# Kernel tuning notes

Hardware: AMD Instinct MI355X
Metric: run time of the kernel (lower is better)

## Reference

```python
import jax, jax.numpy as jnp
import numpy as np

N_NODES = 100000
N_EDGES = 1600000
N_FEAT = 128
N_CLASSES = 64
K_HOPS = 2


def setup_inputs() -> dict:
    key = jax.random.key(0)
    k1, k2, k3 = jax.random.split(key, 3)
    x = jax.random.normal(k1, (N_NODES, N_FEAT), dtype=jnp.float32)
    edge_index = jax.random.randint(k2, (2, N_EDGES), 0, N_NODES, dtype=jnp.int64)
    # Linear layer params (PyG Linear: y = x @ W.T + b)
    lim = 1.0 / np.sqrt(N_FEAT)
    W = jax.random.uniform(k3, (N_CLASSES, N_FEAT), dtype=jnp.float32, minval=-lim, maxval=lim)
    b = jnp.zeros((N_CLASSES,), dtype=jnp.float32)
    return {"x": x, "edge_index": edge_index, "W": W, "b": b}


def _gcn_norm(edge_index, num_nodes):
    # Add self-loops with weight 1 (PyG gcn_norm default)
    loops = jnp.arange(num_nodes, dtype=edge_index.dtype)
    row = jnp.concatenate([edge_index[0], loops])
    col = jnp.concatenate([edge_index[1], loops])
    ew = jnp.ones(row.shape[0], dtype=jnp.float32)
    deg = jax.ops.segment_sum(ew, col, num_segments=num_nodes)
    dinv = jnp.where(deg > 0, jax.lax.rsqrt(deg), 0.0)
    norm = dinv[row] * ew * dinv[col]  # [E + N]
    return row, col, norm


def reference(x, edge_index, W, b):
    n = x.shape[0]
    row, col, norm = _gcn_norm(edge_index, n)
    # K rounds of normalized SpMM: out[col] += norm * x[row]
    for _ in range(K_HOPS):
        x = jax.ops.segment_sum(norm[:, None] * x[row], col, num_segments=n)
    # Final linear
    return x @ W.T + b
```

## Files before the change

### kernel.cpp

```cpp
#include <hip/hip_runtime.h>
#include <hip/hip_fp16.h>

#define NFEAT 128
#define NCLS  64
#define CPB   192
#define SCAP  3600
#define NBMAX 544
#define PCHUNK 2048

typedef _Float16 f16;
typedef __attribute__((ext_vector_type(8))) _Float16 f16x8;
typedef __attribute__((ext_vector_type(4))) float f32x4;

__global__ __launch_bounds__(256) void part_k(const int* __restrict__ row,
                                              const int* __restrict__ col, int E,
                                              int* __restrict__ bcursor,
                                              int* __restrict__ ebuf, int NB) {
    __shared__ int ecol[PCHUNK];
    __shared__ int h[NBMAX];
    __shared__ int cur[NBMAX];
    int t = threadIdx.x;
    int start = blockIdx.x * PCHUNK;
    int end   = min(start + PCHUNK, E);
    int cnt_c = end - start;
    for (int i = t; i < NB; i += 256) h[i] = 0;
    for (int k = t; k < cnt_c; k += 256) ecol[k] = col[start + k];
    __syncthreads();
    for (int k = t; k < cnt_c; k += 256)
        atomicAdd(&h[ecol[k] / CPB], 1);
    __syncthreads();
    for (int i = t; i < NB; i += 256)
        cur[i] = i * SCAP + (h[i] ? atomicAdd(&bcursor[i], h[i]) : 0);
    __syncthreads();
    for (int k = t; k < cnt_c; k += 256) {
        int c = ecol[k], b = c / CPB, cl = c - b * CPB;
        int pos = atomicAdd(&cur[b], 1);
        if (pos < (b + 1) * SCAP)
            ebuf[pos] = row[start + k] | (cl << 17);
    }
}

__global__ __launch_bounds__(256) void sort_k(const int* __restrict__ ebuf,
                                              const int* __restrict__ bcursor,
                                              float* __restrict__ dinv,
                                              int2* __restrict__ pc,
                                              int* __restrict__ csr, int N) {
    __shared__ int sld[SCAP];
    __shared__ int h[CPB];
    __shared__ int cur[CPB];
    __shared__ int sc[256];
    int b = blockIdx.x, t = threadIdx.x;
    int base = b * SCAP;
    int cntb = min(bcursor[b], SCAP);
    for (int i = t; i < CPB; i += 256) h[i] = 0;
    for (int j = t; j < cntb; j += 256) sld[j] = ebuf[base + j];
    __syncthreads();
    for (int j = t; j < cntb; j += 256)
        atomicAdd(&h[sld[j] >> 17], 1);
    __syncthreads();
    int v = (t < CPB) ? h[t] : 0;
    sc[t] = v;
    for (int off = 1; off < 256; off <<= 1) {
        __syncthreads();
        int a = (t >= off) ? sc[t - off] : 0;
        __syncthreads();
        sc[t] += a;
    }
    __syncthreads();
    if (t < CPB) {
        int c = b * CPB + t;
        int p = base + sc[t] - v;
        cur[t] = p;
        if (c < N) {
            pc[c] = make_int2(p, v);
            dinv[c] = rsqrtf((float)(v + 1));
        }
    }
    __syncthreads();
    for (int j = t; j < cntb; j += 256) {
        int e = sld[j];
        int pos = atomicAdd(&cur[e >> 17], 1);
        csr[pos] = e & 0x1FFFF;
    }
}

__global__ __launch_bounds__(256) void proj_k(const float* __restrict__ x,
                                              const float* __restrict__ W,
                                              const float* __restrict__ dinv,
                                              f16* __restrict__ z, int n) {
    __shared__ __align__(16) f16 zbuf[4][16][64];
    int t = threadIdx.x;
    int w = t >> 6, l = t & 63;
    int lr = l & 15;
    int lk = l >> 4;

    f16x8 bfrag[4][4];
#pragma unroll
    for (int ct = 0; ct < 4; ++ct)
#pragma unroll
        for (int m = 0; m < 4; ++m) {
            const float* wp = &W[(size_t)(ct * 16 + lr) * NFEAT + m * 32 + lk * 8];
            float4 w0 = *reinterpret_cast<const float4*>(wp);
            float4 w1 = *reinterpret_cast<const float4*>(wp + 4);
            f16x8 bb;
            bb[0] = (f16)w0.x; bb[1] = (f16)w0.y; bb[2] = (f16)w0.z; bb[3] = (f16)w0.w;
            bb[4] = (f16)w1.x; bb[5] = (f16)w1.y; bb[6] = (f16)w1.z; bb[7] = (f16)w1.w;
            bfrag[ct][m] = bb;
        }

    int nb = blockIdx.x * 64 + w * 16;
    int arow = nb + lr;
    bool aok = arow < n;
    const float* xp = &x[(size_t)(aok ? arow : 0) * NFEAT + lk * 8];

    f32x4 acc[4];
#pragma unroll
    for (int ct = 0; ct < 4; ++ct) acc[ct] = (f32x4){0.f, 0.f, 0.f, 0.f};

#pragma unroll
    for (int m = 0; m < 4; ++m) {
        float4 x0 = make_float4(0.f, 0.f, 0.f, 0.f);
        float4 x1 = make_float4(0.f, 0.f, 0.f, 0.f);
        if (aok) {
            x0 = *reinterpret_cast<const float4*>(xp + m * 32);
            x1 = *reinterpret_cast<const float4*>(xp + m * 32 + 4);
        }
        f16x8 a;
        a[0] = (f16)x0.x; a[1] = (f16)x0.y; a[2] = (f16)x0.z; a[3] = (f16)x0.w;
        a[4] = (f16)x1.x; a[5] = (f16)x1.y; a[6] = (f16)x1.z; a[7] = (f16)x1.w;
#pragma unroll
        for (int ct = 0; ct < 4; ++ct)
            acc[ct] = __builtin_amdgcn_mfma_f32_16x16x32_f16(a, bfrag[ct][m], acc[ct], 0, 0, 0);
    }

    float d[4];
#pragma unroll
    for (int r = 0; r < 4; ++r) {
        int node = nb + lk * 4 + r;
        d[r] = (node < n) ? dinv[node] : 0.f;
    }
#pragma unroll
    for (int ct = 0; ct < 4; ++ct)
#pragma unroll
        for (int r = 0; r < 4; ++r)
            zbuf[w][lk * 4 + r][ct * 16 + lr] = (f16)(acc[ct][r] * d[r]);
    __builtin_amdgcn_s_waitcnt(0);

    const uint4* zb = reinterpret_cast<const uint4*>(&zbuf[w][0][0]);
    uint4 v0 = zb[l * 2], v1 = zb[l * 2 + 1];
    int node = nb + (l >> 2);
    if (node < n) {
        uint4* op = reinterpret_cast<uint4*>(&z[(size_t)node * NCLS + (l & 3) * 16]);
        op[0] = v0; op[1] = v1;
    }
}

template <int FINAL>
__global__ __launch_bounds__(256) void spmm_k(const __half* __restrict__ zin,
                                              void* __restrict__ outp,
                                              const int2* __restrict__ pc,
                                              const float* __restrict__ dinv,
                                              const int* __restrict__ csr,
                                              const float* __restrict__ bias, int n) {
    int t = threadIdx.x;
    int lane = t & 63;
    int wid  = blockIdx.x * 4 + (t >> 6);
    wid = __builtin_amdgcn_readfirstlane(wid);
    if (wid >= n) return;

    int sub = lane >> 3;
    int cg  = (lane & 7) * 8;
    int2 se = pc[wid];
    int s = se.x, e = s + se.y;

    float a[8];
#pragma unroll
    for (int k = 0; k < 8; ++k) a[k] = 0.f;

#define ACCUM(u)                                                            \
    {                                                                       \
        __half2 t0 = *reinterpret_cast<const __half2*>(&u.x);               \
        __half2 t1 = *reinterpret_cast<const __half2*>(&u.y);               \
        __half2 t2 = *reinterpret_cast<const __half2*>(&u.z);               \
        __half2 t3 = *reinterpret_cast<const __half2*>(&u.w);               \
        float2 f0 = __half22float2(t0), f1 = __half22float2(t1);            \
        float2 f2 = __half22float2(t2), f3 = __half22float2(t3);            \
        a[0] += f0.x; a[1] += f0.y; a[2] += f1.x; a[3] += f1.y;             \
        a[4] += f2.x; a[5] += f2.y; a[6] += f3.x; a[7] += f3.y;             \
    }

    int j = s;
    int rA = 0, rB = 0;
    if (j + 16 <= e) { rA = csr[j + sub]; rB = csr[j + 8 + sub]; }
    while (j + 16 <= e) {
        int r0 = rA, r1 = rB;
        int jn = j + 16;
        if (jn + 16 <= e) { rA = csr[jn + sub]; rB = csr[jn + 8 + sub]; }
        uint4 g0 = *reinterpret_cast<const uint4*>(&zin[(size_t)r0 * NCLS + cg]);
        uint4 g1 = *reinterpret_cast<const uint4*>(&zin[(size_t)r1 * NCLS + cg]);
        ACCUM(g0); ACCUM(g1);
        j = jn;
    }
    if (j + 8 <= e) {
        int r0 = csr[j + sub];
        uint4 g0 = *reinterpret_cast<const uint4*>(&zin[(size_t)r0 * NCLS + cg]);
        ACCUM(g0);
        j += 8;
    }
    if (j + sub < e) {
        int r0 = csr[j + sub];
        uint4 g0 = *reinterpret_cast<const uint4*>(&zin[(size_t)r0 * NCLS + cg]);
        ACCUM(g0);
    }

#pragma unroll
    for (int m = 8; m <= 32; m <<= 1)
#pragma unroll
        for (int k = 0; k < 8; ++k)
            a[k] += __shfl_xor(a[k], m, 64);

    uint4 sv = *reinterpret_cast<const uint4*>(&zin[(size_t)wid * NCLS + cg]);
    ACCUM(sv);
#undef ACCUM

    float d = dinv[wid];
    if (FINAL) {
        float* out = (float*)outp;
        float4 b0 = *reinterpret_cast<const float4*>(&bias[cg]);
        float4 b1 = *reinterpret_cast<const float4*>(&bias[cg + 4]);
        if (sub == 0) {
            float4 o0, o1;
            o0.x = fmaf(d, a[0], b0.x); o0.y = fmaf(d, a[1], b0.y);
            o0.z = fmaf(d, a[2], b0.z); o0.w = fmaf(d, a[3], b0.w);
            o1.x = fmaf(d, a[4], b1.x); o1.y = fmaf(d, a[5], b1.y);
            o1.z = fmaf(d, a[6], b1.z); o1.w = fmaf(d, a[7], b1.w);
            *reinterpret_cast<float4*>(&out[(size_t)wid * NCLS + cg])     = o0;
            *reinterpret_cast<float4*>(&out[(size_t)wid * NCLS + cg + 4]) = o1;
        }
    } else {
        __half* zo = (__half*)outp;
        float d2 = d * d;
        if (sub == 0) {
            __half2 h0 = __floats2half2_rn(d2 * a[0], d2 * a[1]);
            __half2 h1 = __floats2half2_rn(d2 * a[2], d2 * a[3]);
            __half2 h2 = __floats2half2_rn(d2 * a[4], d2 * a[5]);
            __half2 h3 = __floats2half2_rn(d2 * a[6], d2 * a[7]);
            uint4 pk;
            pk.x = *reinterpret_cast<unsigned int*>(&h0);
            pk.y = *reinterpret_cast<unsigned int*>(&h1);
            pk.z = *reinterpret_cast<unsigned int*>(&h2);
            pk.w = *reinterpret_cast<unsigned int*>(&h3);
            *reinterpret_cast<uint4*>(&zo[(size_t)wid * NCLS + cg]) = pk;
        }
    }
}

extern "C" void kernel_launch(void* const* d_in, const int* in_sizes, int n_in,
                              void* d_out, int out_size, void* d_ws, size_t ws_size,
                              hipStream_t stream) {
    const float* x  = (const float*)d_in[0];
    const int*   ei = (const int*)d_in[1];
    const float* W  = (const float*)d_in[2];
    const float* b  = (const float*)d_in[3];

    const int N = in_sizes[0] / NFEAT;
    const int E = in_sizes[1] / 2;
    const int* row = ei;
    const int* col = ei + E;
    const int NB = (N + CPB - 1) / CPB;
    if (NB > NBMAX) return;

    const size_t SLOTS = (size_t)NB * SCAP;
    f16*   z0      = (f16*)d_ws;
    f16*   z1      = z0 + (size_t)N * NCLS;
    int*   ebuf    = (int*)(z1 + (size_t)N * NCLS);
    int*   csr     = ebuf + SLOTS;
    float* dinv    = (float*)(csr + SLOTS);
    int2*  pc      = (int2*)(dinv + N);
    int*   bcursor = (int*)(pc + N);

    size_t needed = (size_t)N * NCLS * 2 * 2
                  + (SLOTS * 2 + (size_t)N * 3 + (size_t)NB) * 4;
    if (ws_size < needed) return;

    hipMemsetAsync(bcursor, 0, (size_t)NB * 4, stream);
    part_k<<<(E + PCHUNK - 1) / PCHUNK, 256, 0, stream>>>(row, col, E, bcursor, ebuf, NB);
    sort_k<<<NB, 256, 0, stream>>>(ebuf, bcursor, dinv, pc, csr, N);

    proj_k<<<(N + 63) / 64, 256, 0, stream>>>(x, W, dinv, z0, N);

    spmm_k<0><<<(N + 3) / 4, 256, 0, stream>>>((const __half*)z0, (void*)z1, pc, dinv, csr, b, N);
    spmm_k<1><<<(N + 3) / 4, 256, 0, stream>>>((const __half*)z1, d_out,     pc, dinv, csr, b, N);
}
```

Measured before the change: 254.7 us.

## Fuse edge partition with projection and move dinv scaling into sort

Edge partitioning and the dense projection now run in one launch, with the first PB blocks partitioning edges and the rest running the MFMA projection without degree scaling. The sort kernel then applies the dinv scale to its block's nodes while it builds the CSR, which removes one kernel launch and lets the two independent stages overlap. Partition chunks grow to 8192 edges per block, and the SpMM gather loop is unrolled to four gathers per iteration with a predicated tail. The cost is an extra read and write of the projected features during scaling, plus higher shared-memory use per block from the larger chunk.

```diff
diff --git a/kernel.cpp b/kernel.cpp
--- a/kernel.cpp
+++ b/kernel.cpp
@@ -6,42 +6,111 @@
 #define CPB   192
 #define SCAP  3600
 #define NBMAX 544
-#define PCHUNK 2048
+#define PCHUNK 8192
 
 typedef _Float16 f16;
 typedef __attribute__((ext_vector_type(8))) _Float16 f16x8;
 typedef __attribute__((ext_vector_type(4))) float f32x4;
 
-__global__ __launch_bounds__(256) void part_k(const int* __restrict__ row,
-                                              const int* __restrict__ col, int E,
-                                              int* __restrict__ bcursor,
-                                              int* __restrict__ ebuf, int NB) {
-    __shared__ int ecol[PCHUNK];
-    __shared__ int h[NBMAX];
-    __shared__ int cur[NBMAX];
+__global__ __launch_bounds__(256) void fat_k(const float* __restrict__ x,
+                                             const float* __restrict__ W,
+                                             const int* __restrict__ row,
+                                             const int* __restrict__ col, int E,
+                                             int* __restrict__ bcursor,
+                                             int* __restrict__ ebuf,
+                                             f16* __restrict__ u0,
+                                             int n, int NB, int PB) {
+    __shared__ union {
+        struct { int ecol[PCHUNK]; int h[NBMAX]; int cur[NBMAX]; } p;
+        __align__(16) f16 zbuf[4][16][64];
+    } sh;
     int t = threadIdx.x;
-    int start = blockIdx.x * PCHUNK;
-    int end   = min(start + PCHUNK, E);
-    int cnt_c = end - start;
-    for (int i = t; i < NB; i += 256) h[i] = 0;
-    for (int k = t; k < cnt_c; k += 256) ecol[k] = col[start + k];
-    __syncthreads();
-    for (int k = t; k < cnt_c; k += 256)
-        atomicAdd(&h[ecol[k] / CPB], 1);
-    __syncthreads();
-    for (int i = t; i < NB; i += 256)
-        cur[i] = i * SCAP + (h[i] ? atomicAdd(&bcursor[i], h[i]) : 0);
-    __syncthreads();
-    for (int k = t; k < cnt_c; k += 256) {
-        int c = ecol[k], b = c / CPB, cl = c - b * CPB;
-        int pos = atomicAdd(&cur[b], 1);
-        if (pos < (b + 1) * SCAP)
-            ebuf[pos] = row[start + k] | (cl << 17);
+
+    if ((int)blockIdx.x < PB) {
+        int start = blockIdx.x * PCHUNK;
+        int end   = min(start + PCHUNK, E);
+        int cnt_c = end - start;
+        for (int i = t; i < NB; i += 256) sh.p.h[i] = 0;
+        for (int k = t; k < cnt_c; k += 256) sh.p.ecol[k] = col[start + k];
+        __syncthreads();
+        for (int k = t; k < cnt_c; k += 256)
+            atomicAdd(&sh.p.h[sh.p.ecol[k] / CPB], 1);
+        __syncthreads();
+        for (int i = t; i < NB; i += 256)
+            sh.p.cur[i] = i * SCAP + (sh.p.h[i] ? atomicAdd(&bcursor[i], sh.p.h[i]) : 0);
+        __syncthreads();
+        for (int k = t; k < cnt_c; k += 256) {
+            int c = sh.p.ecol[k], b = c / CPB, cl = c - b * CPB;
+            int pos = atomicAdd(&sh.p.cur[b], 1);
+            if (pos < (b + 1) * SCAP)
+                ebuf[pos] = row[start + k] | (cl << 17);
+        }
+        return;
+    }
+
+    int w = t >> 6, l = t & 63;
+    int lr = l & 15;
+    int lk = l >> 4;
+
+    f16x8 bfrag[4][4];
+#pragma unroll
+    for (int ct = 0; ct < 4; ++ct)
+#pragma unroll
+        for (int m = 0; m < 4; ++m) {
+            const float* wp = &W[(size_t)(ct * 16 + lr) * NFEAT + m * 32 + lk * 8];
+            float4 w0 = *reinterpret_cast<const float4*>(wp);
+            float4 w1 = *reinterpret_cast<const float4*>(wp + 4);
+            f16x8 bb;
+            bb[0] = (f16)w0.x; bb[1] = (f16)w0.y; bb[2] = (f16)w0.z; bb[3] = (f16)w0.w;
+            bb[4] = (f16)w1.x; bb[5] = (f16)w1.y; bb[6] = (f16)w1.z; bb[7] = (f16)w1.w;
+            bfrag[ct][m] = bb;
+        }
+
+    int nb = (blockIdx.x - PB) * 64 + w * 16;
+    int arow = nb + lr;
+    bool aok = arow < n;
+    const float* xp = &x[(size_t)(aok ? arow : 0) * NFEAT + lk * 8];
+
+    f32x4 acc[4];
+#pragma unroll
+    for (int ct = 0; ct < 4; ++ct) acc[ct] = (f32x4){0.f, 0.f, 0.f, 0.f};
+
+#pragma unroll
+    for (int m = 0; m < 4; ++m) {
+        float4 x0 = make_float4(0.f, 0.f, 0.f, 0.f);
+        float4 x1 = make_float4(0.f, 0.f, 0.f, 0.f);
+        if (aok) {
+            x0 = *reinterpret_cast<const float4*>(xp + m * 32);
+            x1 = *reinterpret_cast<const float4*>(xp + m * 32 + 4);
+        }
+        f16x8 a;
+        a[0] = (f16)x0.x; a[1] = (f16)x0.y; a[2] = (f16)x0.z; a[3] = (f16)x0.w;
+        a[4] = (f16)x1.x; a[5] = (f16)x1.y; a[6] = (f16)x1.z; a[7] = (f16)x1.w;
+#pragma unroll
+        for (int ct = 0; ct < 4; ++ct)
+            acc[ct] = __builtin_amdgcn_mfma_f32_16x16x32_f16(a, bfrag[ct][m], acc[ct], 0, 0, 0);
+    }
+
+#pragma unroll
+    for (int ct = 0; ct < 4; ++ct)
+#pragma unroll
+        for (int r = 0; r < 4; ++r)
+            sh.zbuf[w][lk * 4 + r][ct * 16 + lr] = (f16)acc[ct][r];
+    __builtin_amdgcn_s_waitcnt(0);
+
+    const uint4* zb = reinterpret_cast<const uint4*>(&sh.zbuf[w][0][0]);
+    uint4 v0 = zb[l * 2], v1 = zb[l * 2 + 1];
+    int node = nb + (l >> 2);
+    if (node < n) {
+        uint4* op = reinterpret_cast<uint4*>(&u0[(size_t)node * NCLS + (l & 3) * 16]);
+        op[0] = v0; op[1] = v1;
     }
 }
 
 __global__ __launch_bounds__(256) void sort_k(const int* __restrict__ ebuf,
                                               const int* __restrict__ bcursor,
+                                              const f16* __restrict__ u0,
+                                              f16* __restrict__ z0,
                                               float* __restrict__ dinv,
                                               int2* __restrict__ pc,
                                               int* __restrict__ csr, int N) {
@@ -49,6 +118,7 @@
     __shared__ int h[CPB];
     __shared__ int cur[CPB];
     __shared__ int sc[256];
+    __shared__ float ds[CPB];
     int b = blockIdx.x, t = threadIdx.x;
     int base = b * SCAP;
     int cntb = min(bcursor[b], SCAP);
@@ -71,9 +141,11 @@
         int c = b * CPB + t;
         int p = base + sc[t] - v;
         cur[t] = p;
+        float d = rsqrtf((float)(v + 1));
+        ds[t] = d;
         if (c < N) {
             pc[c] = make_int2(p, v);
-            dinv[c] = rsqrtf((float)(v + 1));
+            dinv[c] = d;
         }
     }
     __syncthreads();
@@ -82,76 +154,22 @@
         int pos = atomicAdd(&cur[e >> 17], 1);
         csr[pos] = e & 0x1FFFF;
     }
-}
-
-__global__ __launch_bounds__(256) void proj_k(const float* __restrict__ x,
-                                              const float* __restrict__ W,
-                                              const float* __restrict__ dinv,
-                                              f16* __restrict__ z, int n) {
-    __shared__ __align__(16) f16 zbuf[4][16][64];
-    int t = threadIdx.x;
-    int w = t >> 6, l = t & 63;
-    int lr = l & 15;
-    int lk = l >> 4;
-
-    f16x8 bfrag[4][4];
-#pragma unroll
-    for (int ct = 0; ct < 4; ++ct)
-#pragma unroll
-        for (int m = 0; m < 4; ++m) {
-            const float* wp = &W[(size_t)(ct * 16 + lr) * NFEAT + m * 32 + lk * 8];
-            float4 w0 = *reinterpret_cast<const float4*>(wp);
-            float4 w1 = *reinterpret_cast<const float4*>(wp + 4);
-            f16x8 bb;
-            bb[0] = (f16)w0.x; bb[1] = (f16)w0.y; bb[2] = (f16)w0.z; bb[3] = (f16)w0.w;
-            bb[4] = (f16)w1.x; bb[5] = (f16)w1.y; bb[6] = (f16)w1.z; bb[7] = (f16)w1.w;
-            bfrag[ct][m] = bb;
-        }
-
-    int nb = blockIdx.x * 64 + w * 16;
-    int arow = nb + lr;
-    bool aok = arow < n;
-    const float* xp = &x[(size_t)(aok ? arow : 0) * NFEAT + lk * 8];
-
-    f32x4 acc[4];
-#pragma unroll
-    for (int ct = 0; ct < 4; ++ct) acc[ct] = (f32x4){0.f, 0.f, 0.f, 0.f};
-
-#pragma unroll
-    for (int m = 0; m < 4; ++m) {
-        float4 x0 = make_float4(0.f, 0.f, 0.f, 0.f);
-        float4 x1 = make_float4(0.f, 0.f, 0.f, 0.f);
-        if (aok) {
-            x0 = *reinterpret_cast<const float4*>(xp + m * 32);
-            x1 = *reinterpret_cast<const float4*>(xp + m * 32 + 4);
-        }
-        f16x8 a;
-        a[0] = (f16)x0.x; a[1] = (f16)x0.y; a[2] = (f16)x0.z; a[3] = (f16)x0.w;
-        a[4] = (f16)x1.x; a[5] = (f16)x1.y; a[6] = (f16)x1.z; a[7] = (f16)x1.w;
-#pragma unroll
-        for (int ct = 0; ct < 4; ++ct)
-            acc[ct] = __builtin_amdgcn_mfma_f32_16x16x32_f16(a, bfrag[ct][m], acc[ct], 0, 0, 0);
-    }
-
-    float d[4];
-#pragma unroll
-    for (int r = 0; r < 4; ++r) {
-        int node = nb + lk * 4 + r;
-        d[r] = (node < n) ? dinv[node] : 0.f;
-    }
-#pragma unroll
-    for (int ct = 0; ct < 4; ++ct)
-#pragma unroll
-        for (int r = 0; r < 4; ++r)
-            zbuf[w][lk * 4 + r][ct * 16 + lr] = (f16)(acc[ct][r] * d[r]);
-    __builtin_amdgcn_s_waitcnt(0);
-
-    const uint4* zb = reinterpret_cast<const uint4*>(&zbuf[w][0][0]);
-    uint4 v0 = zb[l * 2], v1 = zb[l * 2 + 1];
-    int node = nb + (l >> 2);
-    if (node < n) {
-        uint4* op = reinterpret_cast<uint4*>(&z[(size_t)node * NCLS + (l & 3) * 16]);
-        op[0] = v0; op[1] = v1;
+    int nodes = min(CPB, N - b * CPB);
+    if (nodes > 0) {
+        const uint4* up = reinterpret_cast<const uint4*>(u0 + (size_t)b * CPB * NCLS);
+        uint4* zp = reinterpret_cast<uint4*>(z0 + (size_t)b * CPB * NCLS);
+        int tot = nodes * 8;
+        for (int i = t; i < tot; i += 256) {
+            float d = ds[i >> 3];
+            uint4 vv = up[i];
+            __half2* hv = reinterpret_cast<__half2*>(&vv);
+#pragma unroll
+            for (int k = 0; k < 4; ++k) {
+                float2 f = __half22float2(hv[k]);
+                hv[k] = __floats2half2_rn(f.x * d, f.y * d);
+            }
+            zp[i] = vv;
+        }
     }
 }
 
@@ -188,30 +206,27 @@
         a[0] += f0.x; a[1] += f0.y; a[2] += f1.x; a[3] += f1.y;             \
         a[4] += f2.x; a[5] += f2.y; a[6] += f3.x; a[7] += f3.y;             \
     }
+#define GATHER(r) (*reinterpret_cast<const uint4*>(&zin[(size_t)(r) * NCLS + cg]))
 
     int j = s;
-    int rA = 0, rB = 0;
-    if (j + 16 <= e) { rA = csr[j + sub]; rB = csr[j + 8 + sub]; }
-    while (j + 16 <= e) {
-        int r0 = rA, r1 = rB;
-        int jn = j + 16;
-        if (jn + 16 <= e) { rA = csr[jn + sub]; rB = csr[jn + 8 + sub]; }
-        uint4 g0 = *reinterpret_cast<const uint4*>(&zin[(size_t)r0 * NCLS + cg]);
-        uint4 g1 = *reinterpret_cast<const uint4*>(&zin[(size_t)r1 * NCLS + cg]);
-        ACCUM(g0); ACCUM(g1);
-        j = jn;
-    }
-    if (j + 8 <= e) {
-        int r0 = csr[j + sub];
-        uint4 g0 = *reinterpret_cast<const uint4*>(&zin[(size_t)r0 * NCLS + cg]);
-        ACCUM(g0);
-        j += 8;
-    }
-    if (j + sub < e) {
-        int r0 = csr[j + sub];
-        uint4 g0 = *reinterpret_cast<const uint4*>(&zin[(size_t)r0 * NCLS + cg]);
-        ACCUM(g0);
-    }
+    while (e - j >= 32) {
+        int r0 = csr[j + sub],      r1 = csr[j + 8 + sub];
+        int r2 = csr[j + 16 + sub], r3 = csr[j + 24 + sub];
+        uint4 g0 = GATHER(r0), g1 = GATHER(r1), g2 = GATHER(r2), g3 = GATHER(r3);
+        ACCUM(g0); ACCUM(g1); ACCUM(g2); ACCUM(g3);
+        j += 32;
+    }
+    int f = (e - j) >> 3;
+    uint4 g0, g1, g2, g3;
+    bool p = (j + f * 8 + sub) < e;
+    if (f > 0) { int r = csr[j + sub];           g0 = GATHER(r); }
+    if (f > 1) { int r = csr[j + 8 + sub];       g1 = GATHER(r); }
+    if (f > 2) { int r = csr[j + 16 + sub];      g2 = GATHER(r); }
+    if (p)     { int r = csr[j + f * 8 + sub];   g3 = GATHER(r); }
+    if (f > 0) ACCUM(g0);
+    if (f > 1) ACCUM(g1);
+    if (f > 2) ACCUM(g2);
+    if (p)     ACCUM(g3);
 
 #pragma unroll
     for (int m = 8; m <= 32; m <<= 1)
@@ -219,8 +234,9 @@
         for (int k = 0; k < 8; ++k)
             a[k] += __shfl_xor(a[k], m, 64);
 
-    uint4 sv = *reinterpret_cast<const uint4*>(&zin[(size_t)wid * NCLS + cg]);
+    uint4 sv = GATHER(wid);
     ACCUM(sv);
+#undef GATHER
 #undef ACCUM
 
     float d = dinv[wid];
@@ -270,10 +286,13 @@
     const int NB = (N + CPB - 1) / CPB;
     if (NB > NBMAX) return;
 
+    const int PB    = (E + PCHUNK - 1) / PCHUNK;
+    const int PROJB = (N + 63) / 64;
+
     const size_t SLOTS = (size_t)NB * SCAP;
-    f16*   z0      = (f16*)d_ws;
-    f16*   z1      = z0 + (size_t)N * NCLS;
-    int*   ebuf    = (int*)(z1 + (size_t)N * NCLS);
+    f16*   u0      = (f16*)d_ws;
+    f16*   z0      = u0 + (size_t)N * NCLS;
+    int*   ebuf    = (int*)(z0 + (size_t)N * NCLS);
     int*   csr     = ebuf + SLOTS;
     float* dinv    = (float*)(csr + SLOTS);
     int2*  pc      = (int2*)(dinv + N);
@@ -284,11 +303,10 @@
     if (ws_size < needed) return;
 
     hipMemsetAsync(bcursor, 0, (size_t)NB * 4, stream);
-    part_k<<<(E + PCHUNK - 1) / PCHUNK, 256, 0, stream>>>(row, col, E, bcursor, ebuf, NB);
-    sort_k<<<NB, 256, 0, stream>>>(ebuf, bcursor, dinv, pc, csr, N);
-
-    proj_k<<<(N + 63) / 64, 256, 0, stream>>>(x, W, dinv, z0, N);
-
+    fat_k<<<PB + PROJB, 256, 0, stream>>>(x, W, row, col, E, bcursor, ebuf, u0, N, NB, PB);
+    sort_k<<<NB, 256, 0, stream>>>(ebuf, bcursor, u0, z0, dinv, pc, csr, N);
+
+    f16* z1 = u0;
     spmm_k<0><<<(N + 3) / 4, 256, 0, stream>>>((const __half*)z0, (void*)z1, pc, dinv, csr, b, N);
     spmm_k<1><<<(N + 3) / 4, 256, 0, stream>>>((const __half*)z1, d_out,     pc, dinv, csr, b, N);
 }
```

Measured after the change: 239.4 us. -6.0%, faster.
